# Kernel optimization log

Hardware: AMD Instinct MI355X
Metric: run time of the kernel (lower is better)

Reference implementation:

```python
import jax, jax.numpy as jnp
import numpy as np


def setup_inputs() -> dict:
    key = jax.random.key(0)
    ks = jax.random.split(key, 5)
    b, c, H, W = 8, 192, 224, 224
    head_dim, p = 32, 7
    nh = c // head_dim
    return {
        "x": jax.random.normal(ks[0], (b, c, H, W), dtype=jnp.float32),
        "w_qkv": jax.random.normal(ks[1], (3 * c, c), dtype=jnp.float32) * 0.02,
        "b_qkv": jnp.zeros((3 * c,), dtype=jnp.float32),
        "rel_pos": jax.random.normal(ks[2], (nh, 2 * p - 1, 2 * p - 1), dtype=jnp.float32) * 0.02,
        "w_out": jax.random.normal(ks[3], (c, c), dtype=jnp.float32) * 0.02,
        "b_out": jnp.zeros((c,), dtype=jnp.float32),
        "window_size": p,
    }


def _rel_bias(rel_pos, p):
    # cord: (p*p, 2) flattened window coordinates (static numpy indices)
    ii, jj = np.meshgrid(np.arange(p), np.arange(p), indexing="ij")
    cord = np.stack([ii.reshape(-1), jj.reshape(-1)], axis=-1)  # (pp, 2)
    rel = cord[:, None, :] - cord[None, :, :] + p - 1  # (pp, pp, 2)
    return rel_pos[:, rel[..., 0], rel[..., 1]]  # (nh, pp, pp)


def reference(x, w_qkv, b_qkv, rel_pos, w_out, b_out, window_size):
    b, c, H, W = x.shape
    p = window_size
    nh = rel_pos.shape[0]
    hd = c // nh
    scale = hd ** -0.5
    w1, w2 = H // p, W // p
    nw, pp = w1 * w2, p * p
    # [b,c,H,W] -> [b,H,W,c] -> windows [b, nw, pp, c]
    xw = jnp.transpose(x, (0, 2, 3, 1))
    xw = xw.reshape(b, w1, p, w2, p, c).transpose(0, 1, 3, 2, 4, 5).reshape(b, nw, pp, c)
    qkv = xw @ w_qkv.T + b_qkv  # [b, nw, pp, 3c]
    qkv = qkv.reshape(b, nw, pp, 3, nh, hd)
    q, k, v = qkv[:, :, :, 0], qkv[:, :, :, 1], qkv[:, :, :, 2]  # [b, nw, pp, nh, hd]
    sim = jnp.einsum("bwphc,bwqhc->bwhpq", q, k) * scale
    sim = sim + _rel_bias(rel_pos, p)[None, None]  # broadcast over b, nw
    probs = jax.nn.softmax(sim, axis=-1)
    out = jnp.einsum("bwhpq,bwqhc->bwphc", probs, v).reshape(b, nw, pp, c)  # (h c) merge
    out = out @ w_out.T + b_out
    out = out.reshape(b, w1, w2, p, p, -1).transpose(0, 1, 3, 2, 4, 5).reshape(b, H, W, -1)
    return jnp.transpose(out, (0, 3, 1, 2))  # [b, c_out, H, W]
```

## Files before the change

### kernel.cpp

```cpp
#include <hip/hip_runtime.h>
#include <hip/hip_bf16.h>

typedef __bf16 bf16x8 __attribute__((ext_vector_type(8)));
typedef float  f32x4  __attribute__((ext_vector_type(4)));

#define NB   8
#define C    192
#define C3   576
#define HH   224
#define WWID 224
#define PW   7
#define NH   6
#define HD   32
#define PP   49
#define MPAD 64

#define XW_LD 200
#define QK_LD 392
#define VT_LD 72
#define PR_LD 72

__global__ void wla_prep(const float* __restrict__ wqkv, const float* __restrict__ wout,
                         const float* __restrict__ relpos,
                         __bf16* __restrict__ wqkv_bf, __bf16* __restrict__ wout_bf,
                         float* __restrict__ bias6) {
  const int n1 = C3 * C, n2 = C * C, n3 = NH * PP * PP;
  for (int i = blockIdx.x * blockDim.x + threadIdx.x; i < n1 + n2 + n3;
       i += gridDim.x * blockDim.x) {
    if (i < n1) {
      wqkv_bf[i] = (__bf16)wqkv[i];
    } else if (i < n1 + n2) {
      wout_bf[i - n1] = (__bf16)wout[i - n1];
    } else {
      int e = i - n1 - n2;
      int h = e / (PP * PP), r = e % (PP * PP);
      int p = r / PP, q = r % PP;
      int di = p / PW - q / PW + (PW - 1);
      int dj = p % PW - q % PW + (PW - 1);
      bias6[e] = relpos[(h * (2 * PW - 1) + di) * (2 * PW - 1) + dj];
    }
  }
}

__global__ __launch_bounds__(512, 2)
void wla_main(const float* __restrict__ x,
              const __bf16* __restrict__ wqkv_bf, const float* __restrict__ bqkv,
              const float* __restrict__ bias6,
              const __bf16* __restrict__ wout_bf, const float* __restrict__ bout,
              float* __restrict__ out) {
  __shared__ __align__(16) __bf16 xw[MPAD * XW_LD];
  __shared__ __align__(16) __bf16 qk[MPAD * QK_LD];
  __shared__ __align__(16) __bf16 vt[NH * HD * VT_LD];
  __shared__ __align__(16) __bf16 pr[8 * 16 * PR_LD];

  const int tid  = threadIdx.x;
  const int lane = tid & 63;
  const int wv   = tid >> 6;
  const int l15  = lane & 15;
  const int lg   = lane >> 4;

  const int blk = blockIdx.x;
  const int bb  = blk >> 10;
  const int wi  = blk & 1023;
  const int wy  = wi >> 5, wx = wi & 31;

  const float* xbase = x + (size_t)bb * C * HH * WWID + (size_t)(wy * PW) * WWID + wx * PW;

  for (int e = tid; e < C * PP; e += 512) {
    int c = e / PP, pos = e - c * PP;
    int py = pos / PW, px = pos - py * PW;
    xw[pos * XW_LD + c] = (__bf16)xbase[(size_t)c * HH * WWID + py * WWID + px];
  }
  for (int e = tid; e < (MPAD - PP) * C; e += 512) {
    int rr = e / C, c = e - rr * C;
    xw[(PP + rr) * XW_LD + c] = (__bf16)0.f;
  }
  __syncthreads();

  {
    f32x4 acc[5][4];
#pragma unroll
    for (int j = 0; j < 5; ++j)
#pragma unroll
      for (int m = 0; m < 4; ++m) acc[j][m] = (f32x4){0.f, 0.f, 0.f, 0.f};

#pragma unroll
    for (int ks = 0; ks < 6; ++ks) {
      bf16x8 af[4];
#pragma unroll
      for (int m = 0; m < 4; ++m)
        af[m] = *(const bf16x8*)(&xw[(m * 16 + l15) * XW_LD + ks * 32 + lg * 8]);
#pragma unroll
      for (int j = 0; j < 5; ++j) {
        int nt = wv + 8 * j;
        bf16x8 bfr = *(const bf16x8*)(wqkv_bf + (size_t)(nt * 16 + l15) * C + ks * 32 + lg * 8);
#pragma unroll
        for (int m = 0; m < 4; ++m)
          acc[j][m] = __builtin_amdgcn_mfma_f32_16x16x32_bf16(af[m], bfr, acc[j][m], 0, 0, 0);
      }
    }
#pragma unroll
    for (int j = 0; j < 5; ++j) {
      int nt = wv + 8 * j;
      if (nt < 36) {
        int cn = nt * 16 + l15;
        float bias = bqkv[cn];
#pragma unroll
        for (int m = 0; m < 4; ++m) {
#pragma unroll
          for (int r = 0; r < 4; ++r) {
            int row = m * 16 + lg * 4 + r;
            float val = acc[j][m][r] + bias;
            if (cn < 2 * C) {
              qk[row * QK_LD + cn] = (__bf16)val;
            } else {
              int hh = (cn - 2 * C) >> 5, d = (cn - 2 * C) & 31;
              vt[(hh * HD + d) * VT_LD + row] = (__bf16)val;
            }
          }
        }
      }
    }
  }
  __syncthreads();

  const float scale = 0.17677669529663687f;
#pragma unroll 1
  for (int u = wv; u < 24; u += 8) {
    int h = u >> 2, qt = u & 3;

    f32x4 s[4];
    {
      bf16x8 aq = *(const bf16x8*)(&qk[(qt * 16 + l15) * QK_LD + h * HD + lg * 8]);
#pragma unroll
      for (int ntj = 0; ntj < 4; ++ntj) {
        bf16x8 bk = *(const bf16x8*)(&qk[(ntj * 16 + l15) * QK_LD + C + h * HD + lg * 8]);
        f32x4 z = (f32x4){0.f, 0.f, 0.f, 0.f};
        s[ntj] = __builtin_amdgcn_mfma_f32_16x16x32_bf16(aq, bk, z, 0, 0, 0);
      }
    }
    const float* bh = bias6 + h * PP * PP;
#pragma unroll
    for (int r = 0; r < 4; ++r) {
      int p = qt * 16 + lg * 4 + r;
      float sv[4];
      float mx = -1e30f;
#pragma unroll
      for (int ntj = 0; ntj < 4; ++ntj) {
        int q = ntj * 16 + l15;
        float v = s[ntj][r] * scale;
        if (p < PP && q < PP) v += bh[p * PP + q];
        if (q >= PP) v = -1e30f;
        sv[ntj] = v;
        mx = fmaxf(mx, v);
      }
#pragma unroll
      for (int d = 1; d < 16; d <<= 1) mx = fmaxf(mx, __shfl_xor(mx, d));
      float ev[4];
      float sum = 0.f;
#pragma unroll
      for (int ntj = 0; ntj < 4; ++ntj) {
        ev[ntj] = __expf(sv[ntj] - mx);
        sum += ev[ntj];
      }
#pragma unroll
      for (int d = 1; d < 16; d <<= 1) sum += __shfl_xor(sum, d);
      float inv = 1.f / sum;
#pragma unroll
      for (int ntj = 0; ntj < 4; ++ntj)
        pr[(wv * 16 + lg * 4 + r) * PR_LD + ntj * 16 + l15] = (__bf16)(ev[ntj] * inv);
    }

    f32x4 o[2];
    o[0] = (f32x4){0.f, 0.f, 0.f, 0.f};
    o[1] = (f32x4){0.f, 0.f, 0.f, 0.f};
#pragma unroll
    for (int ks = 0; ks < 2; ++ks) {
      bf16x8 ap = *(const bf16x8*)(&pr[(wv * 16 + l15) * PR_LD + ks * 32 + lg * 8]);
#pragma unroll
      for (int ntj = 0; ntj < 2; ++ntj) {
        bf16x8 bv = *(const bf16x8*)(&vt[(h * HD + ntj * 16 + l15) * VT_LD + ks * 32 + lg * 8]);
        o[ntj] = __builtin_amdgcn_mfma_f32_16x16x32_bf16(ap, bv, o[ntj], 0, 0, 0);
      }
    }
#pragma unroll
    for (int ntj = 0; ntj < 2; ++ntj)
#pragma unroll
      for (int r = 0; r < 4; ++r)
        xw[(qt * 16 + lg * 4 + r) * XW_LD + h * HD + ntj * 16 + l15] = (__bf16)o[ntj][r];
  }
  __syncthreads();

  {
    int mh  = wv >> 2;
    int nt0 = (wv & 3) * 3;
    f32x4 acc[3][2];
#pragma unroll
    for (int j = 0; j < 3; ++j)
#pragma unroll
      for (int mm = 0; mm < 2; ++mm) acc[j][mm] = (f32x4){0.f, 0.f, 0.f, 0.f};

#pragma unroll
    for (int ks = 0; ks < 6; ++ks) {
      bf16x8 af[2];
#pragma unroll
      for (int mm = 0; mm < 2; ++mm)
        af[mm] = *(const bf16x8*)(&xw[((mh * 2 + mm) * 16 + l15) * XW_LD + ks * 32 + lg * 8]);
#pragma unroll
      for (int j = 0; j < 3; ++j) {
        int cn = (nt0 + j) * 16 + l15;
        bf16x8 bfr = *(const bf16x8*)(wout_bf + (size_t)cn * C + ks * 32 + lg * 8);
#pragma unroll
        for (int mm = 0; mm < 2; ++mm)
          acc[j][mm] = __builtin_amdgcn_mfma_f32_16x16x32_bf16(af[mm], bfr, acc[j][mm], 0, 0, 0);
      }
    }
#pragma unroll
    for (int j = 0; j < 3; ++j) {
      int cn = (nt0 + j) * 16 + l15;
      float bias = bout[cn];
      float* obase = out + ((size_t)bb * C + cn) * HH * WWID + (size_t)(wy * PW) * WWID + wx * PW;
#pragma unroll
      for (int mm = 0; mm < 2; ++mm) {
#pragma unroll
        for (int r = 0; r < 4; ++r) {
          int row = (mh * 2 + mm) * 16 + lg * 4 + r;
          if (row < PP) {
            int py = row / PW, px = row - py * PW;
            obase[py * WWID + px] = acc[j][mm][r] + bias;
          }
        }
      }
    }
  }
}

extern "C" void kernel_launch(void* const* d_in, const int* in_sizes, int n_in,
                              void* d_out, int out_size, void* d_ws, size_t ws_size,
                              hipStream_t stream) {
  const float* x    = (const float*)d_in[0];
  const float* wqkv = (const float*)d_in[1];
  const float* bqkv = (const float*)d_in[2];
  const float* relp = (const float*)d_in[3];
  const float* wout = (const float*)d_in[4];
  const float* bout = (const float*)d_in[5];
  float* outp = (float*)d_out;

  __bf16* wqkv_bf = (__bf16*)d_ws;
  __bf16* wout_bf = wqkv_bf + (size_t)C3 * C;
  float*  bias6   = (float*)(wout_bf + (size_t)C * C);

  wla_prep<<<dim3(128), dim3(256), 0, stream>>>(wqkv, wout, relp, wqkv_bf, wout_bf, bias6);
  wla_main<<<dim3(NB * 1024), dim3(512), 0, stream>>>(x, wqkv_bf, bqkv, bias6, wout_bf, bout, outp);
}
```

Measured before the change: 1.779 ms.

## Pre-transpose input to bf16 NHWC and read QKV operands directly from global

Adds a transpose kernel that converts x from fp32 NCHW to bf16 channel-last in the workspace. The main kernel then loads GEMM A fragments straight from global instead of staging a strided gather through LDS. The main kernel also splits q/k into separate buffers, keeps softmax probabilities in registers and reuses the q buffer for them, which shrinks LDS and raises the occupancy hint from 2 to 4 blocks. The cost is an extra full-tensor pass through HBM (fp32 read plus bf16 write and reread). It falls back to the old kernel when the workspace is too small.

```diff
diff --git a/kernel.cpp b/kernel.cpp
--- a/kernel.cpp
+++ b/kernel.cpp
@@ -3,22 +3,29 @@
 
 typedef __bf16 bf16x8 __attribute__((ext_vector_type(8)));
 typedef float  f32x4  __attribute__((ext_vector_type(4)));
+typedef unsigned short u16x8 __attribute__((ext_vector_type(8)));
 
 #define NB   8
 #define C    192
 #define C3   576
 #define HH   224
 #define WWID 224
+#define HW   50176
 #define PW   7
 #define NH   6
 #define HD   32
 #define PP   49
 #define MPAD 64
 
-#define XW_LD 200
-#define QK_LD 392
+#define Q_LD  200
 #define VT_LD 72
 #define PR_LD 72
+
+static __device__ __forceinline__ unsigned int pack2bf(float a, float b) {
+  union { __bf16 h[2]; unsigned int u; } x;
+  x.h[0] = (__bf16)a; x.h[1] = (__bf16)b;
+  return x.u;
+}
 
 __global__ void wla_prep(const float* __restrict__ wqkv, const float* __restrict__ wout,
                          const float* __restrict__ relpos,
@@ -42,16 +49,46 @@
   }
 }
 
-__global__ __launch_bounds__(512, 2)
-void wla_main(const float* __restrict__ x,
+__global__ __launch_bounds__(256)
+void wla_tr(const float* __restrict__ x, __bf16* __restrict__ xT) {
+  __shared__ unsigned int tl[C * 33];
+  const int t = threadIdx.x;
+  const int bidb = blockIdx.x / 784;
+  const int tile = blockIdx.x % 784;
+  const size_t pix0 = (size_t)tile * 64;
+
+#pragma unroll
+  for (int p = 0; p < 12; ++p) {
+    int c = p * 16 + (t >> 4);
+    int px0 = (t & 15) * 4;
+    const float4 v = *(const float4*)(x + ((size_t)(bidb * C + c)) * HW + pix0 + px0);
+    tl[c * 33 + (px0 >> 1)]     = pack2bf(v.x, v.y);
+    tl[c * 33 + (px0 >> 1) + 1] = pack2bf(v.z, v.w);
+  }
+  __syncthreads();
+
+  const int px = t >> 2, seg = t & 3;
+  const unsigned short* tls = (const unsigned short*)tl;
+  __bf16* obase = xT + ((size_t)bidb * HW + pix0 + px) * C;
+#pragma unroll
+  for (int s = 0; s < 6; ++s) {
+    int c0 = seg * 48 + s * 8;
+    u16x8 a;
+#pragma unroll
+    for (int i = 0; i < 8; ++i) a[i] = tls[(c0 + i) * 66 + px];
+    *(u16x8*)((unsigned short*)obase + c0) = a;
+  }
+}
+
+__global__ __launch_bounds__(512, 4)
+void wla_main(const __bf16* __restrict__ xT,
               const __bf16* __restrict__ wqkv_bf, const float* __restrict__ bqkv,
               const float* __restrict__ bias6,
               const __bf16* __restrict__ wout_bf, const float* __restrict__ bout,
               float* __restrict__ out) {
-  __shared__ __align__(16) __bf16 xw[MPAD * XW_LD];
-  __shared__ __align__(16) __bf16 qk[MPAD * QK_LD];
+  __shared__ __align__(16) __bf16 qbuf[MPAD * Q_LD];
+  __shared__ __align__(16) __bf16 kbuf[MPAD * Q_LD];
   __shared__ __align__(16) __bf16 vt[NH * HD * VT_LD];
-  __shared__ __align__(16) __bf16 pr[8 * 16 * PR_LD];
 
   const int tid  = threadIdx.x;
   const int lane = tid & 63;
@@ -64,6 +101,224 @@
   const int wi  = blk & 1023;
   const int wy  = wi >> 5, wx = wi & 31;
 
+  const __bf16* aptr[4];
+#pragma unroll
+  for (int m = 0; m < 4; ++m) {
+    int T = m * 16 + l15;
+    int py = T / 7, px = T - py * 7;
+    int pix = (wy * PW + py) * WWID + wx * PW + px;
+    if (T >= PP) pix = 0;
+    aptr[m] = xT + ((size_t)bb * HW + pix) * C;
+  }
+
+  {
+    f32x4 acc[5][4];
+#pragma unroll
+    for (int j = 0; j < 5; ++j)
+#pragma unroll
+      for (int m = 0; m < 4; ++m) acc[j][m] = (f32x4){0.f, 0.f, 0.f, 0.f};
+
+#pragma unroll
+    for (int ks = 0; ks < 6; ++ks) {
+      bf16x8 af[4];
+#pragma unroll
+      for (int m = 0; m < 4; ++m)
+        af[m] = *(const bf16x8*)(aptr[m] + ks * 32 + lg * 8);
+#pragma unroll
+      for (int j = 0; j < 5; ++j) {
+        int nt = wv + 8 * j;
+        bf16x8 bfr = *(const bf16x8*)(wqkv_bf + (size_t)(nt * 16 + l15) * C + ks * 32 + lg * 8);
+#pragma unroll
+        for (int m = 0; m < 4; ++m)
+          acc[j][m] = __builtin_amdgcn_mfma_f32_16x16x32_bf16(af[m], bfr, acc[j][m], 0, 0, 0);
+      }
+    }
+#pragma unroll
+    for (int j = 0; j < 5; ++j) {
+      int nt = wv + 8 * j;
+      if (nt < 36) {
+        int cn = nt * 16 + l15;
+        float bias = bqkv[cn];
+#pragma unroll
+        for (int m = 0; m < 4; ++m) {
+#pragma unroll
+          for (int r = 0; r < 4; ++r) {
+            int row = m * 16 + lg * 4 + r;
+            float val = acc[j][m][r] + bias;
+            if (cn < C) {
+              qbuf[row * Q_LD + cn] = (__bf16)val;
+            } else if (cn < 2 * C) {
+              kbuf[row * Q_LD + (cn - C)] = (__bf16)val;
+            } else {
+              vt[(cn - 2 * C) * VT_LD + row] = (__bf16)val;
+            }
+          }
+        }
+      }
+    }
+  }
+  __syncthreads();
+
+  const float scale = 0.17677669529663687f;
+  unsigned int pregs[3][8];
+#pragma unroll
+  for (int uu = 0; uu < 3; ++uu) {
+    int u = uu * 8 + wv;
+    int h = u >> 2, qt = u & 3;
+
+    f32x4 s[4];
+    {
+      bf16x8 aq = *(const bf16x8*)(&qbuf[(qt * 16 + l15) * Q_LD + h * HD + lg * 8]);
+#pragma unroll
+      for (int ntj = 0; ntj < 4; ++ntj) {
+        bf16x8 bk = *(const bf16x8*)(&kbuf[(ntj * 16 + l15) * Q_LD + h * HD + lg * 8]);
+        f32x4 z = (f32x4){0.f, 0.f, 0.f, 0.f};
+        s[ntj] = __builtin_amdgcn_mfma_f32_16x16x32_bf16(aq, bk, z, 0, 0, 0);
+      }
+    }
+    const float* bh = bias6 + h * PP * PP;
+    float pf[4][4];
+#pragma unroll
+    for (int r = 0; r < 4; ++r) {
+      int p = qt * 16 + lg * 4 + r;
+      float sv[4];
+      float mx = -1e30f;
+#pragma unroll
+      for (int ntj = 0; ntj < 4; ++ntj) {
+        int q = ntj * 16 + l15;
+        float v = s[ntj][r] * scale;
+        if (p < PP && q < PP) v += bh[p * PP + q];
+        if (q >= PP) v = -1e30f;
+        sv[ntj] = v;
+        mx = fmaxf(mx, v);
+      }
+#pragma unroll
+      for (int d = 1; d < 16; d <<= 1) mx = fmaxf(mx, __shfl_xor(mx, d));
+      float ev[4];
+      float sum = 0.f;
+#pragma unroll
+      for (int ntj = 0; ntj < 4; ++ntj) {
+        ev[ntj] = __expf(sv[ntj] - mx);
+        sum += ev[ntj];
+      }
+#pragma unroll
+      for (int d = 1; d < 16; d <<= 1) sum += __shfl_xor(sum, d);
+      float inv = 1.f / sum;
+#pragma unroll
+      for (int ntj = 0; ntj < 4; ++ntj) pf[r][ntj] = ev[ntj] * inv;
+    }
+#pragma unroll
+    for (int ntj = 0; ntj < 4; ++ntj)
+#pragma unroll
+      for (int rr = 0; rr < 2; ++rr)
+        pregs[uu][ntj * 2 + rr] = pack2bf(pf[rr * 2][ntj], pf[rr * 2 + 1][ntj]);
+  }
+  __syncthreads();
+
+#pragma unroll
+  for (int uu = 0; uu < 3; ++uu) {
+    int u = uu * 8 + wv;
+    int h = u >> 2, qt = u & 3;
+    unsigned short* pr = (unsigned short*)qbuf + wv * 16 * PR_LD;
+
+#pragma unroll
+    for (int ntj = 0; ntj < 4; ++ntj)
+#pragma unroll
+      for (int r = 0; r < 4; ++r) {
+        unsigned int pk = pregs[uu][ntj * 2 + (r >> 1)];
+        pr[(lg * 4 + r) * PR_LD + ntj * 16 + l15] =
+            (unsigned short)(pk >> ((r & 1) * 16));
+      }
+
+    f32x4 o[2];
+    o[0] = (f32x4){0.f, 0.f, 0.f, 0.f};
+    o[1] = (f32x4){0.f, 0.f, 0.f, 0.f};
+#pragma unroll
+    for (int ks = 0; ks < 2; ++ks) {
+      bf16x8 ap = *(const bf16x8*)((const __bf16*)qbuf + wv * 16 * PR_LD + l15 * PR_LD + ks * 32 + lg * 8);
+#pragma unroll
+      for (int ntj = 0; ntj < 2; ++ntj) {
+        bf16x8 bv = *(const bf16x8*)(&vt[(h * HD + ntj * 16 + l15) * VT_LD + ks * 32 + lg * 8]);
+        o[ntj] = __builtin_amdgcn_mfma_f32_16x16x32_bf16(ap, bv, o[ntj], 0, 0, 0);
+      }
+    }
+#pragma unroll
+    for (int ntj = 0; ntj < 2; ++ntj)
+#pragma unroll
+      for (int r = 0; r < 4; ++r)
+        kbuf[(qt * 16 + lg * 4 + r) * Q_LD + h * HD + ntj * 16 + l15] = (__bf16)o[ntj][r];
+  }
+  __syncthreads();
+
+  {
+    int mh  = wv >> 2;
+    int nt0 = (wv & 3) * 3;
+    f32x4 acc[3][2];
+#pragma unroll
+    for (int j = 0; j < 3; ++j)
+#pragma unroll
+      for (int mm = 0; mm < 2; ++mm) acc[j][mm] = (f32x4){0.f, 0.f, 0.f, 0.f};
+
+#pragma unroll
+    for (int ks = 0; ks < 6; ++ks) {
+      bf16x8 af[2];
+#pragma unroll
+      for (int mm = 0; mm < 2; ++mm)
+        af[mm] = *(const bf16x8*)(&kbuf[((mh * 2 + mm) * 16 + l15) * Q_LD + ks * 32 + lg * 8]);
+#pragma unroll
+      for (int j = 0; j < 3; ++j) {
+        int cn = (nt0 + j) * 16 + l15;
+        bf16x8 bfr = *(const bf16x8*)(wout_bf + (size_t)cn * C + ks * 32 + lg * 8);
+#pragma unroll
+        for (int mm = 0; mm < 2; ++mm)
+          acc[j][mm] = __builtin_amdgcn_mfma_f32_16x16x32_bf16(af[mm], bfr, acc[j][mm], 0, 0, 0);
+      }
+    }
+#pragma unroll
+    for (int j = 0; j < 3; ++j) {
+      int cn = (nt0 + j) * 16 + l15;
+      float bias = bout[cn];
+      float* obase = out + ((size_t)bb * C + cn) * HW + (size_t)(wy * PW) * WWID + wx * PW;
+#pragma unroll
+      for (int mm = 0; mm < 2; ++mm) {
+#pragma unroll
+        for (int r = 0; r < 4; ++r) {
+          int row = (mh * 2 + mm) * 16 + lg * 4 + r;
+          if (row < PP) {
+            int py = row / PW, px = row - py * PW;
+            obase[py * WWID + px] = acc[j][mm][r] + bias;
+          }
+        }
+      }
+    }
+  }
+}
+
+#define XW_LD 200
+#define QK_LD 392
+
+__global__ __launch_bounds__(512, 2)
+void wla_main_v1(const float* __restrict__ x,
+                 const __bf16* __restrict__ wqkv_bf, const float* __restrict__ bqkv,
+                 const float* __restrict__ bias6,
+                 const __bf16* __restrict__ wout_bf, const float* __restrict__ bout,
+                 float* __restrict__ out) {
+  __shared__ __align__(16) __bf16 xw[MPAD * XW_LD];
+  __shared__ __align__(16) __bf16 qk[MPAD * QK_LD];
+  __shared__ __align__(16) __bf16 vt[NH * HD * VT_LD];
+  __shared__ __align__(16) __bf16 pr[8 * 16 * PR_LD];
+
+  const int tid  = threadIdx.x;
+  const int lane = tid & 63;
+  const int wv   = tid >> 6;
+  const int l15  = lane & 15;
+  const int lg   = lane >> 4;
+
+  const int blk = blockIdx.x;
+  const int bb  = blk >> 10;
+  const int wi  = blk & 1023;
+  const int wy  = wi >> 5, wx = wi & 31;
+
   const float* xbase = x + (size_t)bb * C * HH * WWID + (size_t)(wy * PW) * WWID + wx * PW;
 
   for (int e = tid; e < C * PP; e += 512) {
@@ -83,7 +338,6 @@
     for (int j = 0; j < 5; ++j)
 #pragma unroll
       for (int m = 0; m < 4; ++m) acc[j][m] = (f32x4){0.f, 0.f, 0.f, 0.f};
-
 #pragma unroll
     for (int ks = 0; ks < 6; ++ks) {
       bf16x8 af[4];
@@ -128,7 +382,6 @@
 #pragma unroll 1
   for (int u = wv; u < 24; u += 8) {
     int h = u >> 2, qt = u & 3;
-
     f32x4 s[4];
     {
       bf16x8 aq = *(const bf16x8*)(&qk[(qt * 16 + l15) * QK_LD + h * HD + lg * 8]);
@@ -170,7 +423,6 @@
       for (int ntj = 0; ntj < 4; ++ntj)
         pr[(wv * 16 + lg * 4 + r) * PR_LD + ntj * 16 + l15] = (__bf16)(ev[ntj] * inv);
     }
-
     f32x4 o[2];
     o[0] = (f32x4){0.f, 0.f, 0.f, 0.f};
     o[1] = (f32x4){0.f, 0.f, 0.f, 0.f};
@@ -199,7 +451,6 @@
     for (int j = 0; j < 3; ++j)
 #pragma unroll
       for (int mm = 0; mm < 2; ++mm) acc[j][mm] = (f32x4){0.f, 0.f, 0.f, 0.f};
-
 #pragma unroll
     for (int ks = 0; ks < 6; ++ks) {
       bf16x8 af[2];
@@ -219,7 +470,7 @@
     for (int j = 0; j < 3; ++j) {
       int cn = (nt0 + j) * 16 + l15;
       float bias = bout[cn];
-      float* obase = out + ((size_t)bb * C + cn) * HH * WWID + (size_t)(wy * PW) * WWID + wx * PW;
+      float* obase = out + ((size_t)bb * C + cn) * HW + (size_t)(wy * PW) * WWID + wx * PW;
 #pragma unroll
       for (int mm = 0; mm < 2; ++mm) {
 #pragma unroll
@@ -250,6 +501,18 @@
   __bf16* wout_bf = wqkv_bf + (size_t)C3 * C;
   float*  bias6   = (float*)(wout_bf + (size_t)C * C);
 
+  const size_t XT_OFF = 524288;
+  const size_t xt_bytes = (size_t)NB * HW * C * 2;
+
   wla_prep<<<dim3(128), dim3(256), 0, stream>>>(wqkv, wout, relp, wqkv_bf, wout_bf, bias6);
-  wla_main<<<dim3(NB * 1024), dim3(512), 0, stream>>>(x, wqkv_bf, bqkv, bias6, wout_bf, bout, outp);
+
+  if (ws_size >= XT_OFF + xt_bytes) {
+    __bf16* xT = (__bf16*)((char*)d_ws + XT_OFF);
+    wla_tr<<<dim3(NB * 784), dim3(256), 0, stream>>>(x, xT);
+    wla_main<<<dim3(NB * 1024), dim3(512), 0, stream>>>(xT, wqkv_bf, bqkv, bias6,
+                                                        wout_bf, bout, outp);
+  } else {
+    wla_main_v1<<<dim3(NB * 1024), dim3(512), 0, stream>>>(x, wqkv_bf, bqkv, bias6,
+                                                           wout_bf, bout, outp);
+  }
 }
```

Result: faster. 1.539 ms (-13.5%).
